# Performance work log

Measured on AMD Instinct MI355X. Metric: run time of the kernel, lower is better.

## Reference

```python
import jax, jax.numpy as jnp
import numpy as np

N = 16384   # total nodes
M = 512     # molecules
D_IN = 64
D_OUT = 64
NEG = -1e9  # mask value for nodes outside a molecule


def setup_inputs() -> dict:
    key = jax.random.key(0)
    ks = jax.random.split(key, 8)
    node_features = jax.random.normal(ks[0], (N, D_IN), dtype=jnp.float32)
    e = jax.random.uniform(ks[1], (N, N), dtype=jnp.float32) * (2.0 / N)
    # molecule membership: sorted segment ids -> one-hot membership matrix
    seg = np.sort(np.asarray(jax.random.randint(ks[2], (N,), 0, M)))
    mnm = (seg[None, :] == np.arange(M)[:, None]).astype(np.float32)
    mol_node_matrix = jnp.asarray(mnm)
    mol_node_mask = jnp.asarray((1.0 - mnm) * NEG)
    s = 1.0 / np.sqrt(D_IN)
    W0 = jax.random.uniform(ks[3], (D_OUT, D_IN), jnp.float32, -s, s)
    b0 = jnp.zeros((D_OUT,), jnp.float32)
    W1 = jax.random.uniform(ks[4], (D_OUT, D_OUT), jnp.float32, -s, s)
    b1 = jnp.zeros((D_OUT,), jnp.float32)
    w2 = jax.random.uniform(ks[5], (1, D_OUT), jnp.float32, -s, s)
    b2 = jnp.zeros((1,), jnp.float32)
    return dict(node_features=node_features, e=e,
                mol_node_matrix=mol_node_matrix, mol_node_mask=mol_node_mask,
                W0=W0, b0=b0, W1=W1, b1=b1, w2=w2, b2=b2)


def reference(node_features, e, mol_node_matrix, mol_node_mask, W0, b0, W1, b1, w2, b2):
    # GraphConvolutionLayer: two linears with adjacency matmul, LeakyReLU between
    h = e @ (node_features @ W0.T + b0)            # [N, D_OUT]
    h = jax.nn.leaky_relu(h, negative_slope=0.01)
    h = e @ (h @ W1.T + b1)                        # [N, D_OUT]
    h = jnp.tanh(h)
    # attention logits per node; mol_node_matrix @ diag(a) == mnm * a^T (broadcast)
    a = (h @ w2.T + b2).reshape(-1)                # [N]
    logits = mol_node_matrix * a[None, :] + mol_node_mask  # [M, N]
    mol_node_weight = jax.nn.softmax(logits, axis=1)
    return mol_node_weight @ h, mol_node_weight
```

## Files before the change

kernel.cpp:

```cpp
#include <hip/hip_runtime.h>
#include <hip/hip_bf16.h>

#define NN 16384
#define MM 512
#define DD 64
#define BK 128
#define BM 32
#define ITERS (NN / BK)
#define BK2 256
#define ITERS2 (NN / BK2)

typedef __attribute__((ext_vector_type(8))) short short8;
typedef __attribute__((ext_vector_type(4))) float f32x4;
typedef __attribute__((ext_vector_type(4))) short short4v;
typedef __attribute__((ext_vector_type(4))) unsigned u32x4;

#define SE 2097152.0f
#define INV_SE 4.76837158203125e-07f

__device__ __forceinline__ short f2bf(float f) {
  union { __hip_bfloat16 b; short s; } u;
  u.b = __float2bfloat16(f);
  return u.s;
}

__device__ __forceinline__ short8 cvt8(f32x4 a, f32x4 b) {
  short8 r;
  r[0] = f2bf(a[0]); r[1] = f2bf(a[1]); r[2] = f2bf(a[2]); r[3] = f2bf(a[3]);
  r[4] = f2bf(b[0]); r[5] = f2bf(b[1]); r[6] = f2bf(b[2]); r[7] = f2bf(b[3]);
  return r;
}

typedef __attribute__((address_space(1))) const unsigned gu32;
typedef __attribute__((address_space(3))) unsigned lu32;
__device__ __forceinline__ void gld16(const void* g, void* l) {
  __builtin_amdgcn_global_load_lds((gu32*)g, (lu32*)l, 16, 0, 0);
}

template <int OFMT>
__global__ __launch_bounds__(256) void linear_mfma(const float* __restrict__ in,
                                                   const float* __restrict__ W,
                                                   const float* __restrict__ b,
                                                   void* __restrict__ xt_) {
  const int t = threadIdx.x, lane = t & 63, w = t >> 6;
  const int rl = lane & 15, hi = lane >> 4;
  const int r0 = blockIdx.x * 64 + w * 16;
  const float* ap = in + (size_t)(r0 + rl) * DD + hi * 8;

  f32x4 acc[4];
#pragma unroll
  for (int g = 0; g < 4; ++g) {
    const float bias = b[g * 16 + rl];
    acc[g][0] = bias; acc[g][1] = bias; acc[g][2] = bias; acc[g][3] = bias;
  }
#pragma unroll
  for (int kk = 0; kk < DD; kk += 32) {
    const short8 af = cvt8(*(const f32x4*)(ap + kk), *(const f32x4*)(ap + kk + 4));
#pragma unroll
    for (int g = 0; g < 4; ++g) {
      const float* wp = W + (size_t)(g * 16 + rl) * DD + hi * 8 + kk;
      const short8 wf = cvt8(*(const f32x4*)wp, *(const f32x4*)(wp + 4));
      acc[g] = __builtin_amdgcn_mfma_f32_16x16x32_bf16(af, wf, acc[g], 0, 0, 0);
    }
  }
#pragma unroll
  for (int g = 0; g < 4; ++g) {
    if (OFMT == 0) {
      unsigned short* xt = (unsigned short*)xt_;
      short4v s;
      s[0] = f2bf(acc[g][0]); s[1] = f2bf(acc[g][1]);
      s[2] = f2bf(acc[g][2]); s[3] = f2bf(acc[g][3]);
      *(short4v*)(xt + (size_t)(g * 16 + rl) * NN + r0 + hi * 4) = s;
    } else {
      unsigned char* xt = (unsigned char*)xt_;
      int pk = __builtin_amdgcn_cvt_pk_fp8_f32(acc[g][0], acc[g][1], 0, false);
      pk = __builtin_amdgcn_cvt_pk_fp8_f32(acc[g][2], acc[g][3], pk, true);
      *(unsigned*)(xt + (size_t)(g * 16 + rl) * NN + r0 + hi * 4) = (unsigned)pk;
    }
  }
}

__global__ __launch_bounds__(256) void gemm1(const float* __restrict__ e,
                                             const unsigned short* __restrict__ xt,
                                             float* __restrict__ out,
                                             unsigned char* __restrict__ e8) {
  __shared__ float Ab[2][BM * BK];
  __shared__ unsigned short Bb[2][64 * BK];
  const int t = threadIdx.x, lane = t & 63, w = t >> 6;
  const int rl = lane & 15, hi = lane >> 4;
  const int wr = w >> 1, wc = w & 1;
  const int r0 = blockIdx.x * BM;
  const int it0 = (blockIdx.x * 37) & (ITERS - 1);

  auto STAGE = [&](int buf, int it) {
    const int k0 = ((it0 + it) & (ITERS - 1)) * BK;
#pragma unroll
    for (int j = 0; j < 4; ++j) {
      const int row = w * 8 + j * 2 + (lane >> 5);
      const float* src =
          e + (size_t)(r0 + row) * NN + k0 + (((lane & 31) ^ (row & 7)) << 2);
      gld16(src, &Ab[buf][(w * 8 + j * 2) * BK]);
    }
#pragma unroll
    for (int j = 0; j < 4; ++j) {
      const int col = w * 16 + j * 4 + (lane >> 4);
      const unsigned short* src =
          xt + (size_t)col * NN + k0 + (((lane & 15) ^ (col & 7)) << 3);
      gld16(src, &Bb[buf][(w * 16 + j * 4) * BK]);
    }
  };

  f32x4 acc[2];
  acc[0][0] = acc[0][1] = acc[0][2] = acc[0][3] = 0.f;
  acc[1][0] = acc[1][1] = acc[1][2] = acc[1][3] = 0.f;

  STAGE(0, 0);
#pragma unroll 1
  for (int it = 0; it < ITERS; ++it) {
    const int cur = it & 1;
    const int k0c = ((it0 + it) & (ITERS - 1)) * BK;
    if (it + 1 < ITERS) {
      STAGE(cur ^ 1, it + 1);
      asm volatile("s_waitcnt vmcnt(9)" ::: "memory");
    } else {
      asm volatile("s_waitcnt vmcnt(0)" ::: "memory");
    }
    __builtin_amdgcn_s_barrier();
    asm volatile("" ::: "memory");
    {
      const int r = t >> 3, j0 = t & 7;
      const float* arow = &Ab[cur][r * BK];
      u32x4 dw;
#pragma unroll
      for (int i = 0; i < 4; ++i) {
        const int c = j0 * 4 + i;
        f32x4 q = *(const f32x4*)&arow[(c ^ (r & 7)) << 2];
        int d = __builtin_amdgcn_cvt_pk_fp8_f32(q[0] * SE, q[1] * SE, 0, false);
        d = __builtin_amdgcn_cvt_pk_fp8_f32(q[2] * SE, q[3] * SE, d, true);
        dw[i] = (unsigned)d;
      }
      *(u32x4*)(e8 + (size_t)(r0 + r) * NN + k0c + j0 * 16) = dw;
    }
#pragma unroll
    for (int kk = 0; kk < BK; kk += 32) {
      const int ca = (kk >> 2) + hi * 2;
      const int arow = (wr * 16 + rl) * BK;
      f32x4 a0 = *(const f32x4*)&Ab[cur][arow + ((ca ^ (rl & 7)) << 2)];
      f32x4 a1 = *(const f32x4*)&Ab[cur][arow + (((ca + 1) ^ (rl & 7)) << 2)];
      const short8 af = cvt8(a0, a1);
      const int cb = (kk >> 3) + hi;
#pragma unroll
      for (int g = 0; g < 2; ++g) {
        const int col = wc * 32 + g * 16 + rl;
        const short8 bf =
            *(const short8*)&Bb[cur][col * BK + ((cb ^ (rl & 7)) << 3)];
        acc[g] = __builtin_amdgcn_mfma_f32_16x16x32_bf16(af, bf, acc[g], 0, 0, 0);
      }
    }
    asm volatile("" ::: "memory");
    __builtin_amdgcn_s_barrier();
  }

#pragma unroll
  for (int g = 0; g < 2; ++g) {
    const int col = wc * 32 + g * 16 + rl;
#pragma unroll
    for (int j = 0; j < 4; ++j) {
      float v = acc[g][j];
      v = (v > 0.f) ? v : 0.01f * v;
      out[(size_t)(r0 + wr * 16 + hi * 4 + j) * DD + col] = v;
    }
  }
}

__global__ __launch_bounds__(256) void gemm2_fp8(const unsigned char* __restrict__ e8,
                                                 const unsigned char* __restrict__ xt8,
                                                 float* __restrict__ out) {
  __shared__ unsigned char Ab2[2][BM * BK2];
  __shared__ unsigned char Bb2[2][64 * BK2];
  const int t = threadIdx.x, lane = t & 63, w = t >> 6;
  const int rl = lane & 15, hi = lane >> 4;
  const int wr = w >> 1, wc = w & 1;
  const int r0 = blockIdx.x * BM;
  const int it0 = (blockIdx.x * 37) & (ITERS2 - 1);

  auto STAGE = [&](int buf, int it) {
    const int k0 = ((it0 + it) & (ITERS2 - 1)) * BK2;
#pragma unroll
    for (int j = 0; j < 2; ++j) {
      const int row = w * 8 + j * 4 + (lane >> 4);
      const unsigned char* src =
          e8 + (size_t)(r0 + row) * NN + k0 + (((lane & 15) ^ (row & 15)) << 4);
      gld16(src, &Ab2[buf][(w * 8 + j * 4) * BK2]);
    }
#pragma unroll
    for (int j = 0; j < 4; ++j) {
      const int col = w * 16 + j * 4 + (lane >> 4);
      const unsigned char* src =
          xt8 + (size_t)col * NN + k0 + (((lane & 15) ^ (col & 15)) << 4);
      gld16(src, &Bb2[buf][(w * 16 + j * 4) * BK2]);
    }
  };

  f32x4 acc[2];
  acc[0][0] = acc[0][1] = acc[0][2] = acc[0][3] = 0.f;
  acc[1][0] = acc[1][1] = acc[1][2] = acc[1][3] = 0.f;

  STAGE(0, 0);
#pragma unroll 1
  for (int it = 0; it < ITERS2; ++it) {
    const int cur = it & 1;
    if (it + 1 < ITERS2) {
      STAGE(cur ^ 1, it + 1);
      asm volatile("s_waitcnt vmcnt(6)" ::: "memory");
    } else {
      asm volatile("s_waitcnt vmcnt(0)" ::: "memory");
    }
    __builtin_amdgcn_s_barrier();
    asm volatile("" ::: "memory");
    const unsigned char* arow = &Ab2[cur][(wr * 16 + rl) * BK2];
#pragma unroll
    for (int kk = 0; kk < BK2; kk += 32) {
      const int ca = (kk >> 4) + (hi >> 1);
      const int off = (hi & 1) * 8;
      const long af = *(const long*)&arow[((ca ^ (rl & 15)) << 4) + off];
#pragma unroll
      for (int g = 0; g < 2; ++g) {
        const int col = wc * 32 + g * 16 + rl;
        const long bf =
            *(const long*)&Bb2[cur][col * BK2 + ((ca ^ (col & 15)) << 4) + off];
        acc[g] = __builtin_amdgcn_mfma_f32_16x16x32_fp8_fp8(af, bf, acc[g], 0, 0, 0);
      }
    }
    asm volatile("" ::: "memory");
    __builtin_amdgcn_s_barrier();
  }

#pragma unroll
  for (int g = 0; g < 2; ++g) {
    const int col = wc * 32 + g * 16 + rl;
#pragma unroll
    for (int j = 0; j < 4; ++j) {
      float v = tanhf(acc[g][j] * INV_SE);
      out[(size_t)(r0 + wr * 16 + hi * 4 + j) * DD + col] = v;
    }
  }
}

__global__ __launch_bounds__(256) void a_kernel(const float* __restrict__ h,
                                                const float* __restrict__ w2,
                                                const float* __restrict__ b2,
                                                float* __restrict__ a) {
  const int t = threadIdx.x;
  const int lane = t & 63;
  const int n = blockIdx.x * 4 + (t >> 6);
  float v = h[(size_t)n * DD + lane] * w2[lane];
#pragma unroll
  for (int off = 32; off > 0; off >>= 1) v += __shfl_xor(v, off);
  if (lane == 0) a[n] = v + b2[0];
}

__global__ __launch_bounds__(256) void softmax_pool(const float* __restrict__ mnm,
                                                    const float* __restrict__ a,
                                                    const float* __restrict__ h,
                                                    float* __restrict__ wout,
                                                    float* __restrict__ out0) {
  __shared__ float red[256];
  __shared__ int redi[256];
  __shared__ float partial[4][64];
  const int m = blockIdx.x, t = threadIdx.x;
  const size_t base = (size_t)m * NN;
  const f32x4* mnm4 = (const f32x4*)(mnm + base);
  const f32x4* a4 = (const f32x4*)a;
  f32x4* wout4 = (f32x4*)(wout + base);

  f32x4 lg[16];
  float mx = -3.0e38f;
  int mn_n = NN, mx_n = -1;
#pragma unroll
  for (int i = 0; i < 16; ++i) {
    const int idx = t + i * 256;
    const f32x4 mv = mnm4[idx];
    const f32x4 av = a4[idx];
    f32x4 v;
#pragma unroll
    for (int j = 0; j < 4; ++j) {
      const bool mem = mv[j] > 0.5f;
      v[j] = mem ? av[j] : -3.0e38f;
      if (mem) {
        const int n = idx * 4 + j;
        mn_n = min(mn_n, n);
        mx_n = max(mx_n, n);
      }
    }
    lg[i] = v;
    mx = fmaxf(mx, fmaxf(fmaxf(v[0], v[1]), fmaxf(v[2], v[3])));
  }
  red[t] = mx; redi[t] = mn_n; __syncthreads();
  for (int s = 128; s > 0; s >>= 1) {
    if (t < s) {
      red[t] = fmaxf(red[t], red[t + s]);
      redi[t] = min(redi[t], redi[t + s]);
    }
    __syncthreads();
  }
  mx = red[0];
  const int ns = redi[0];
  __syncthreads();
  redi[t] = mx_n; __syncthreads();
  for (int s = 128; s > 0; s >>= 1) {
    if (t < s) redi[t] = max(redi[t], redi[t + s]);
    __syncthreads();
  }
  const int ne = redi[0];
  __syncthreads();

  const bool empty = (ne < 0);
  float sm = 0.f;
#pragma unroll
  for (int i = 0; i < 16; ++i) {
    f32x4 v = lg[i];
#pragma unroll
    for (int j = 0; j < 4; ++j)
      v[j] = empty ? 1.0f : ((v[j] > -1.0e38f) ? expf(v[j] - mx) : 0.0f);
    lg[i] = v;
    sm += v[0] + v[1] + v[2] + v[3];
  }
  red[t] = sm; __syncthreads();
  for (int s = 128; s > 0; s >>= 1) {
    if (t < s) red[t] += red[t + s];
    __syncthreads();
  }
  const float inv = 1.0f / red[0];
#pragma unroll
  for (int i = 0; i < 16; ++i) wout4[t + i * 256] = lg[i] * inv;

  __threadfence_block();
  __syncthreads();

  const int s0 = empty ? 0 : ns;
  const int e0 = empty ? NN : ne + 1;
  const int d = t & 63, sub = t >> 6;
  const float* wrow = wout + base;
  float accp = 0.f;
  for (int n = s0 + sub; n < e0; n += 4)
    accp += wrow[n] * h[(size_t)n * DD + d];
  partial[sub][d] = accp;
  __syncthreads();
  if (t < 64)
    out0[m * DD + t] =
        partial[0][t] + partial[1][t] + partial[2][t] + partial[3][t];
}

extern "C" void kernel_launch(void* const* d_in, const int* in_sizes, int n_in,
                              void* d_out, int out_size, void* d_ws, size_t ws_size,
                              hipStream_t stream) {
  const float* nf  = (const float*)d_in[0];
  const float* e   = (const float*)d_in[1];
  const float* mnm = (const float*)d_in[2];
  const float* W0  = (const float*)d_in[4];
  const float* b0  = (const float*)d_in[5];
  const float* W1  = (const float*)d_in[6];
  const float* b1  = (const float*)d_in[7];
  const float* w2  = (const float*)d_in[8];
  const float* b2  = (const float*)d_in[9];

  char* ws = (char*)d_ws;
  unsigned short* XT0 = (unsigned short*)(ws);
  unsigned char*  XT8 = (unsigned char*)(ws + (size_t)2 * 1024 * 1024);
  float* h1 = (float*)(ws + (size_t)4 * 1024 * 1024);
  float* h  = (float*)(ws + (size_t)8 * 1024 * 1024);
  float* av = (float*)(ws + (size_t)12 * 1024 * 1024);
  unsigned char* e8 = (unsigned char*)(ws + (size_t)16 * 1024 * 1024);

  float* out0 = (float*)d_out;
  float* wout = out0 + (size_t)MM * DD;

  linear_mfma<0><<<256, 256, 0, stream>>>(nf, W0, b0, XT0);
  gemm1<<<512, 256, 0, stream>>>(e, XT0, h1, e8);
  linear_mfma<1><<<256, 256, 0, stream>>>(h1, W1, b1, XT8);
  gemm2_fp8<<<512, 256, 0, stream>>>(e8, XT8, h);
  a_kernel<<<4096, 256, 0, stream>>>(h, w2, b2, av);
  softmax_pool<<<512, 256, 0, stream>>>(mnm, av, h, wout, out0);
}
```

Measured before the change: 383.9 us.

## Load B operand directly from global into registers, bypassing LDS

Both adjacency GEMM kernels stop staging the small transposed B matrix (xt / xt8) through shared memory. Each wave now loads its MFMA B fragments straight from global memory into double-buffered registers, with the loop unrolled by two to alternate register buffers. This removes LDS traffic and shared memory for B, which may raise occupancy. In exchange it adds register pressure, non-coalesced 16/8-byte global loads, and depends on hand-tuned vmcnt wait counts.

```diff
diff --git a/kernel.cpp b/kernel.cpp
--- a/kernel.cpp
+++ b/kernel.cpp
@@ -85,14 +85,16 @@
                                              float* __restrict__ out,
                                              unsigned char* __restrict__ e8) {
   __shared__ float Ab[2][BM * BK];
-  __shared__ unsigned short Bb[2][64 * BK];
   const int t = threadIdx.x, lane = t & 63, w = t >> 6;
   const int rl = lane & 15, hi = lane >> 4;
   const int wr = w >> 1, wc = w & 1;
   const int r0 = blockIdx.x * BM;
   const int it0 = (blockIdx.x * 37) & (ITERS - 1);
 
-  auto STAGE = [&](int buf, int it) {
+  const unsigned short* bp0 = xt + (size_t)(wc * 32 + rl) * NN + hi * 8;
+  const unsigned short* bp1 = xt + (size_t)(wc * 32 + 16 + rl) * NN + hi * 8;
+
+  auto STAGE_A = [&](int buf, int it) {
     const int k0 = ((it0 + it) & (ITERS - 1)) * BK;
 #pragma unroll
     for (int j = 0; j < 4; ++j) {
@@ -101,12 +103,15 @@
           e + (size_t)(r0 + row) * NN + k0 + (((lane & 31) ^ (row & 7)) << 2);
       gld16(src, &Ab[buf][(w * 8 + j * 2) * BK]);
     }
-#pragma unroll
-    for (int j = 0; j < 4; ++j) {
-      const int col = w * 16 + j * 4 + (lane >> 4);
-      const unsigned short* src =
-          xt + (size_t)col * NN + k0 + (((lane & 15) ^ (col & 7)) << 3);
-      gld16(src, &Bb[buf][(w * 16 + j * 4) * BK]);
+  };
+
+  short8 bA[8], bB[8];
+  auto LOADB = [&](short8* dst, int it) {
+    const int k0 = ((it0 + it) & (ITERS - 1)) * BK;
+#pragma unroll
+    for (int kki = 0; kki < 4; ++kki) {
+      dst[kki] = *(const short8*)(bp0 + k0 + kki * 32);
+      dst[4 + kki] = *(const short8*)(bp1 + k0 + kki * 32);
     }
   };
 
@@ -114,52 +119,52 @@
   acc[0][0] = acc[0][1] = acc[0][2] = acc[0][3] = 0.f;
   acc[1][0] = acc[1][1] = acc[1][2] = acc[1][3] = 0.f;
 
-  STAGE(0, 0);
+#define G1BODY(CUR, BCUR, BNXT, IT)                                            \
+  {                                                                            \
+    const int k0c = ((it0 + (IT)) & (ITERS - 1)) * BK;                         \
+    if ((IT) + 1 < ITERS) {                                                    \
+      STAGE_A((CUR) ^ 1, (IT) + 1);                                            \
+      LOADB(BNXT, (IT) + 1);                                                   \
+      asm volatile("s_waitcnt vmcnt(12)" ::: "memory");                        \
+    } else {                                                                   \
+      asm volatile("s_waitcnt vmcnt(0)" ::: "memory");                         \
+    }                                                                          \
+    __builtin_amdgcn_s_barrier();                                              \
+    asm volatile("" ::: "memory");                                             \
+    {                                                                          \
+      const int r = t >> 3, j0 = t & 7;                                        \
+      const float* arw = &Ab[CUR][r * BK];                                     \
+      u32x4 dw;                                                                \
+      _Pragma("unroll") for (int i = 0; i < 4; ++i) {                          \
+        const int c = j0 * 4 + i;                                              \
+        f32x4 q = *(const f32x4*)&arw[(c ^ (r & 7)) << 2];                     \
+        int d2 = __builtin_amdgcn_cvt_pk_fp8_f32(q[0] * SE, q[1] * SE, 0, false); \
+        d2 = __builtin_amdgcn_cvt_pk_fp8_f32(q[2] * SE, q[3] * SE, d2, true);  \
+        dw[i] = (unsigned)d2;                                                  \
+      }                                                                        \
+      *(u32x4*)(e8 + (size_t)(r0 + r) * NN + k0c + j0 * 16) = dw;              \
+    }                                                                          \
+    _Pragma("unroll") for (int kk = 0; kk < BK; kk += 32) {                    \
+      const int ca = (kk >> 2) + hi * 2;                                       \
+      const int arow = (wr * 16 + rl) * BK;                                    \
+      f32x4 a0 = *(const f32x4*)&Ab[CUR][arow + ((ca ^ (rl & 7)) << 2)];       \
+      f32x4 a1 = *(const f32x4*)&Ab[CUR][arow + (((ca + 1) ^ (rl & 7)) << 2)]; \
+      const short8 af = cvt8(a0, a1);                                          \
+      acc[0] = __builtin_amdgcn_mfma_f32_16x16x32_bf16(af, (BCUR)[kk >> 5], acc[0], 0, 0, 0);     \
+      acc[1] = __builtin_amdgcn_mfma_f32_16x16x32_bf16(af, (BCUR)[4 + (kk >> 5)], acc[1], 0, 0, 0); \
+    }                                                                          \
+    asm volatile("" ::: "memory");                                             \
+    __builtin_amdgcn_s_barrier();                                              \
+  }
+
+  STAGE_A(0, 0);
+  LOADB(bA, 0);
 #pragma unroll 1
-  for (int it = 0; it < ITERS; ++it) {
-    const int cur = it & 1;
-    const int k0c = ((it0 + it) & (ITERS - 1)) * BK;
-    if (it + 1 < ITERS) {
-      STAGE(cur ^ 1, it + 1);
-      asm volatile("s_waitcnt vmcnt(9)" ::: "memory");
-    } else {
-      asm volatile("s_waitcnt vmcnt(0)" ::: "memory");
-    }
-    __builtin_amdgcn_s_barrier();
-    asm volatile("" ::: "memory");
-    {
-      const int r = t >> 3, j0 = t & 7;
-      const float* arow = &Ab[cur][r * BK];
-      u32x4 dw;
-#pragma unroll
-      for (int i = 0; i < 4; ++i) {
-        const int c = j0 * 4 + i;
-        f32x4 q = *(const f32x4*)&arow[(c ^ (r & 7)) << 2];
-        int d = __builtin_amdgcn_cvt_pk_fp8_f32(q[0] * SE, q[1] * SE, 0, false);
-        d = __builtin_amdgcn_cvt_pk_fp8_f32(q[2] * SE, q[3] * SE, d, true);
-        dw[i] = (unsigned)d;
-      }
-      *(u32x4*)(e8 + (size_t)(r0 + r) * NN + k0c + j0 * 16) = dw;
-    }
-#pragma unroll
-    for (int kk = 0; kk < BK; kk += 32) {
-      const int ca = (kk >> 2) + hi * 2;
-      const int arow = (wr * 16 + rl) * BK;
-      f32x4 a0 = *(const f32x4*)&Ab[cur][arow + ((ca ^ (rl & 7)) << 2)];
-      f32x4 a1 = *(const f32x4*)&Ab[cur][arow + (((ca + 1) ^ (rl & 7)) << 2)];
-      const short8 af = cvt8(a0, a1);
-      const int cb = (kk >> 3) + hi;
-#pragma unroll
-      for (int g = 0; g < 2; ++g) {
-        const int col = wc * 32 + g * 16 + rl;
-        const short8 bf =
-            *(const short8*)&Bb[cur][col * BK + ((cb ^ (rl & 7)) << 3)];
-        acc[g] = __builtin_amdgcn_mfma_f32_16x16x32_bf16(af, bf, acc[g], 0, 0, 0);
-      }
-    }
-    asm volatile("" ::: "memory");
-    __builtin_amdgcn_s_barrier();
-  }
+  for (int it = 0; it < ITERS; it += 2) {
+    G1BODY(0, bA, bB, it);
+    G1BODY(1, bB, bA, it + 1);
+  }
+#undef G1BODY
 
 #pragma unroll
   for (int g = 0; g < 2; ++g) {
@@ -177,14 +182,16 @@
                                                  const unsigned char* __restrict__ xt8,
                                                  float* __restrict__ out) {
   __shared__ unsigned char Ab2[2][BM * BK2];
-  __shared__ unsigned char Bb2[2][64 * BK2];
   const int t = threadIdx.x, lane = t & 63, w = t >> 6;
   const int rl = lane & 15, hi = lane >> 4;
   const int wr = w >> 1, wc = w & 1;
   const int r0 = blockIdx.x * BM;
   const int it0 = (blockIdx.x * 37) & (ITERS2 - 1);
 
-  auto STAGE = [&](int buf, int it) {
+  const unsigned char* bq0 = xt8 + (size_t)(wc * 32 + rl) * NN + hi * 8;
+  const unsigned char* bq1 = xt8 + (size_t)(wc * 32 + 16 + rl) * NN + hi * 8;
+
+  auto STAGE_A = [&](int buf, int it) {
     const int k0 = ((it0 + it) & (ITERS2 - 1)) * BK2;
 #pragma unroll
     for (int j = 0; j < 2; ++j) {
@@ -193,12 +200,15 @@
           e8 + (size_t)(r0 + row) * NN + k0 + (((lane & 15) ^ (row & 15)) << 4);
       gld16(src, &Ab2[buf][(w * 8 + j * 4) * BK2]);
     }
-#pragma unroll
-    for (int j = 0; j < 4; ++j) {
-      const int col = w * 16 + j * 4 + (lane >> 4);
-      const unsigned char* src =
-          xt8 + (size_t)col * NN + k0 + (((lane & 15) ^ (col & 15)) << 4);
-      gld16(src, &Bb2[buf][(w * 16 + j * 4) * BK2]);
+  };
+
+  long bA[16], bB[16];
+  auto LOADB = [&](long* dst, int it) {
+    const int k0 = ((it0 + it) & (ITERS2 - 1)) * BK2;
+#pragma unroll
+    for (int kki = 0; kki < 8; ++kki) {
+      dst[kki] = *(const long*)(bq0 + k0 + kki * 32);
+      dst[8 + kki] = *(const long*)(bq1 + k0 + kki * 32);
     }
   };
 
@@ -206,35 +216,37 @@
   acc[0][0] = acc[0][1] = acc[0][2] = acc[0][3] = 0.f;
   acc[1][0] = acc[1][1] = acc[1][2] = acc[1][3] = 0.f;
 
-  STAGE(0, 0);
+#define G2BODY(CUR, BCUR, BNXT, IT)                                            \
+  {                                                                            \
+    if ((IT) + 1 < ITERS2) {                                                   \
+      STAGE_A((CUR) ^ 1, (IT) + 1);                                            \
+      LOADB(BNXT, (IT) + 1);                                                   \
+      asm volatile("s_waitcnt vmcnt(18)" ::: "memory");                        \
+    } else {                                                                   \
+      asm volatile("s_waitcnt vmcnt(0)" ::: "memory");                         \
+    }                                                                          \
+    __builtin_amdgcn_s_barrier();                                              \
+    asm volatile("" ::: "memory");                                             \
+    const unsigned char* arw = &Ab2[CUR][(wr * 16 + rl) * BK2];                \
+    _Pragma("unroll") for (int kk = 0; kk < BK2; kk += 32) {                   \
+      const int ca = (kk >> 4) + (hi >> 1);                                    \
+      const int off = (hi & 1) * 8;                                            \
+      const long af = *(const long*)&arw[((ca ^ (rl & 15)) << 4) + off];       \
+      acc[0] = __builtin_amdgcn_mfma_f32_16x16x32_fp8_fp8(af, (BCUR)[kk >> 5], acc[0], 0, 0, 0);      \
+      acc[1] = __builtin_amdgcn_mfma_f32_16x16x32_fp8_fp8(af, (BCUR)[8 + (kk >> 5)], acc[1], 0, 0, 0); \
+    }                                                                          \
+    asm volatile("" ::: "memory");                                             \
+    __builtin_amdgcn_s_barrier();                                              \
+  }
+
+  STAGE_A(0, 0);
+  LOADB(bA, 0);
 #pragma unroll 1
-  for (int it = 0; it < ITERS2; ++it) {
-    const int cur = it & 1;
-    if (it + 1 < ITERS2) {
-      STAGE(cur ^ 1, it + 1);
-      asm volatile("s_waitcnt vmcnt(6)" ::: "memory");
-    } else {
-      asm volatile("s_waitcnt vmcnt(0)" ::: "memory");
-    }
-    __builtin_amdgcn_s_barrier();
-    asm volatile("" ::: "memory");
-    const unsigned char* arow = &Ab2[cur][(wr * 16 + rl) * BK2];
-#pragma unroll
-    for (int kk = 0; kk < BK2; kk += 32) {
-      const int ca = (kk >> 4) + (hi >> 1);
-      const int off = (hi & 1) * 8;
-      const long af = *(const long*)&arow[((ca ^ (rl & 15)) << 4) + off];
-#pragma unroll
-      for (int g = 0; g < 2; ++g) {
-        const int col = wc * 32 + g * 16 + rl;
-        const long bf =
-            *(const long*)&Bb2[cur][col * BK2 + ((ca ^ (col & 15)) << 4) + off];
-        acc[g] = __builtin_amdgcn_mfma_f32_16x16x32_fp8_fp8(af, bf, acc[g], 0, 0, 0);
-      }
-    }
-    asm volatile("" ::: "memory");
-    __builtin_amdgcn_s_barrier();
-  }
+  for (int it = 0; it < ITERS2; it += 2) {
+    G2BODY(0, bA, bB, it);
+    G2BODY(1, bB, bA, it + 1);
+  }
+#undef G2BODY
 
 #pragma unroll
   for (int g = 0; g < 2; ++g) {
```

After: 619.4 us. 61.3% more time.

## Halve row tile to 16 and double grid for both adjacency GEMMs

Applied to the files above, without the earlier changes.

Shrinks the per-block row tile of both large GEMMs from 32 to 16 rows. Each of the four waves now owns one 16-column slice, and the grid grows from 512 to 1024 blocks, so there are more blocks than the 256 CUs can hold at once and more waves to hide memory latency. Staging, the fp8 conversion of e, the wait counts and the epilogue are all re-mapped to match. The cost is that the B operand (the XT matrix) is reloaded twice as often across blocks, and each wave issues fewer MFMAs per barrier.

```diff
diff --git a/kernel.cpp b/kernel.cpp
--- a/kernel.cpp
+++ b/kernel.cpp
@@ -5,7 +5,7 @@
 #define MM 512
 #define DD 64
 #define BK 128
-#define BM 32
+#define BM 16
 #define ITERS (NN / BK)
 #define BK2 256
 #define ITERS2 (NN / BK2)
@@ -13,7 +13,7 @@
 typedef __attribute__((ext_vector_type(8))) short short8;
 typedef __attribute__((ext_vector_type(4))) float f32x4;
 typedef __attribute__((ext_vector_type(4))) short short4v;
-typedef __attribute__((ext_vector_type(4))) unsigned u32x4;
+typedef __attribute__((ext_vector_type(2))) unsigned u32x2;
 
 #define SE 2097152.0f
 #define INV_SE 4.76837158203125e-07f
@@ -88,18 +88,17 @@
   __shared__ unsigned short Bb[2][64 * BK];
   const int t = threadIdx.x, lane = t & 63, w = t >> 6;
   const int rl = lane & 15, hi = lane >> 4;
-  const int wr = w >> 1, wc = w & 1;
   const int r0 = blockIdx.x * BM;
   const int it0 = (blockIdx.x * 37) & (ITERS - 1);
 
   auto STAGE = [&](int buf, int it) {
     const int k0 = ((it0 + it) & (ITERS - 1)) * BK;
 #pragma unroll
-    for (int j = 0; j < 4; ++j) {
-      const int row = w * 8 + j * 2 + (lane >> 5);
+    for (int j = 0; j < 2; ++j) {
+      const int row = w * 4 + j * 2 + (lane >> 5);
       const float* src =
           e + (size_t)(r0 + row) * NN + k0 + (((lane & 31) ^ (row & 7)) << 2);
-      gld16(src, &Ab[buf][(w * 8 + j * 2) * BK]);
+      gld16(src, &Ab[buf][(w * 4 + j * 2) * BK]);
     }
 #pragma unroll
     for (int j = 0; j < 4; ++j) {
@@ -110,9 +109,8 @@
     }
   };
 
-  f32x4 acc[2];
-  acc[0][0] = acc[0][1] = acc[0][2] = acc[0][3] = 0.f;
-  acc[1][0] = acc[1][1] = acc[1][2] = acc[1][3] = 0.f;
+  f32x4 acc;
+  acc[0] = acc[1] = acc[2] = acc[3] = 0.f;
 
   STAGE(0, 0);
 #pragma unroll 1
@@ -121,54 +119,50 @@
     const int k0c = ((it0 + it) & (ITERS - 1)) * BK;
     if (it + 1 < ITERS) {
       STAGE(cur ^ 1, it + 1);
-      asm volatile("s_waitcnt vmcnt(9)" ::: "memory");
+      asm volatile("s_waitcnt vmcnt(6)" ::: "memory");
     } else {
       asm volatile("s_waitcnt vmcnt(0)" ::: "memory");
     }
     __builtin_amdgcn_s_barrier();
     asm volatile("" ::: "memory");
     {
-      const int r = t >> 3, j0 = t & 7;
-      const float* arow = &Ab[cur][r * BK];
-      u32x4 dw;
-#pragma unroll
-      for (int i = 0; i < 4; ++i) {
-        const int c = j0 * 4 + i;
-        f32x4 q = *(const f32x4*)&arow[(c ^ (r & 7)) << 2];
-        int d = __builtin_amdgcn_cvt_pk_fp8_f32(q[0] * SE, q[1] * SE, 0, false);
-        d = __builtin_amdgcn_cvt_pk_fp8_f32(q[2] * SE, q[3] * SE, d, true);
-        dw[i] = (unsigned)d;
+      const int r = t >> 4, j0 = t & 15;
+      const float* arw = &Ab[cur][r * BK];
+      u32x2 dw;
+#pragma unroll
+      for (int i = 0; i < 2; ++i) {
+        const int c = j0 * 2 + i;
+        f32x4 q = *(const f32x4*)&arw[(c ^ (r & 7)) << 2];
+        int d2 = __builtin_amdgcn_cvt_pk_fp8_f32(q[0] * SE, q[1] * SE, 0, false);
+        d2 = __builtin_amdgcn_cvt_pk_fp8_f32(q[2] * SE, q[3] * SE, d2, true);
+        dw[i] = (unsigned)d2;
       }
-      *(u32x4*)(e8 + (size_t)(r0 + r) * NN + k0c + j0 * 16) = dw;
+      *(u32x2*)(e8 + (size_t)(r0 + r) * NN + k0c + j0 * 8) = dw;
     }
 #pragma unroll
     for (int kk = 0; kk < BK; kk += 32) {
       const int ca = (kk >> 2) + hi * 2;
-      const int arow = (wr * 16 + rl) * BK;
+      const int arow = rl * BK;
       f32x4 a0 = *(const f32x4*)&Ab[cur][arow + ((ca ^ (rl & 7)) << 2)];
       f32x4 a1 = *(const f32x4*)&Ab[cur][arow + (((ca + 1) ^ (rl & 7)) << 2)];
       const short8 af = cvt8(a0, a1);
       const int cb = (kk >> 3) + hi;
-#pragma unroll
-      for (int g = 0; g < 2; ++g) {
-        const int col = wc * 32 + g * 16 + rl;
-        const short8 bf =
-            *(const short8*)&Bb[cur][col * BK + ((cb ^ (rl & 7)) << 3)];
-        acc[g] = __builtin_amdgcn_mfma_f32_16x16x32_bf16(af, bf, acc[g], 0, 0, 0);
-      }
+      const int col = w * 16 + rl;
+      const short8 bf =
+          *(const short8*)&Bb[cur][col * BK + ((cb ^ (rl & 7)) << 3)];
+      acc = __builtin_amdgcn_mfma_f32_16x16x32_bf16(af, bf, acc, 0, 0, 0);
     }
     asm volatile("" ::: "memory");
     __builtin_amdgcn_s_barrier();
   }
 
-#pragma unroll
-  for (int g = 0; g < 2; ++g) {
-    const int col = wc * 32 + g * 16 + rl;
-#pragma unroll
-    for (int j = 0; j < 4; ++j) {
-      float v = acc[g][j];
+  {
+    const int col = w * 16 + rl;
+#pragma unroll
+    for (int j = 0; j < 4; ++j) {
+      float v = acc[j];
       v = (v > 0.f) ? v : 0.01f * v;
-      out[(size_t)(r0 + wr * 16 + hi * 4 + j) * DD + col] = v;
+      out[(size_t)(r0 + hi * 4 + j) * DD + col] = v;
     }
   }
 }
@@ -180,18 +174,16 @@
   __shared__ unsigned char Bb2[2][64 * BK2];
   const int t = threadIdx.x, lane = t & 63, w = t >> 6;
   const int rl = lane & 15, hi = lane >> 4;
-  const int wr = w >> 1, wc = w & 1;
   const int r0 = blockIdx.x * BM;
   const int it0 = (blockIdx.x * 37) & (ITERS2 - 1);
 
   auto STAGE = [&](int buf, int it) {
     const int k0 = ((it0 + it) & (ITERS2 - 1)) * BK2;
-#pragma unroll
-    for (int j = 0; j < 2; ++j) {
-      const int row = w * 8 + j * 4 + (lane >> 4);
+    {
+      const int row = w * 4 + (lane >> 4);
       const unsigned char* src =
           e8 + (size_t)(r0 + row) * NN + k0 + (((lane & 15) ^ (row & 15)) << 4);
-      gld16(src, &Ab2[buf][(w * 8 + j * 4) * BK2]);
+      gld16(src, &Ab2[buf][w * 4 * BK2]);
     }
 #pragma unroll
     for (int j = 0; j < 4; ++j) {
@@ -202,9 +194,8 @@
     }
   };
 
-  f32x4 acc[2];
-  acc[0][0] = acc[0][1] = acc[0][2] = acc[0][3] = 0.f;
-  acc[1][0] = acc[1][1] = acc[1][2] = acc[1][3] = 0.f;
+  f32x4 acc;
+  acc[0] = acc[1] = acc[2] = acc[3] = 0.f;
 
   STAGE(0, 0);
 #pragma unroll 1
@@ -212,37 +203,33 @@
     const int cur = it & 1;
     if (it + 1 < ITERS2) {
       STAGE(cur ^ 1, it + 1);
-      asm volatile("s_waitcnt vmcnt(6)" ::: "memory");
+      asm volatile("s_waitcnt vmcnt(5)" ::: "memory");
     } else {
       asm volatile("s_waitcnt vmcnt(0)" ::: "memory");
     }
     __builtin_amdgcn_s_barrier();
     asm volatile("" ::: "memory");
-    const unsigned char* arow = &Ab2[cur][(wr * 16 + rl) * BK2];
+    const unsigned char* arw = &Ab2[cur][rl * BK2];
 #pragma unroll
     for (int kk = 0; kk < BK2; kk += 32) {
       const int ca = (kk >> 4) + (hi >> 1);
       const int off = (hi & 1) * 8;
-      const long af = *(const long*)&arow[((ca ^ (rl & 15)) << 4) + off];
-#pragma unroll
-      for (int g = 0; g < 2; ++g) {
-        const int col = wc * 32 + g * 16 + rl;
-        const long bf =
-            *(const long*)&Bb2[cur][col * BK2 + ((ca ^ (col & 15)) << 4) + off];
-        acc[g] = __builtin_amdgcn_mfma_f32_16x16x32_fp8_fp8(af, bf, acc[g], 0, 0, 0);
-      }
+      const long af = *(const long*)&arw[((ca ^ (rl & 15)) << 4) + off];
+      const int col = w * 16 + rl;
+      const long bf =
+          *(const long*)&Bb2[cur][col * BK2 + ((ca ^ (rl & 15)) << 4) + off];
+      acc = __builtin_amdgcn_mfma_f32_16x16x32_fp8_fp8(af, bf, acc, 0, 0, 0);
     }
     asm volatile("" ::: "memory");
     __builtin_amdgcn_s_barrier();
   }
 
-#pragma unroll
-  for (int g = 0; g < 2; ++g) {
-    const int col = wc * 32 + g * 16 + rl;
-#pragma unroll
-    for (int j = 0; j < 4; ++j) {
-      float v = tanhf(acc[g][j] * INV_SE);
-      out[(size_t)(r0 + wr * 16 + hi * 4 + j) * DD + col] = v;
+  {
+    const int col = w * 16 + rl;
+#pragma unroll
+    for (int j = 0; j < 4; ++j) {
+      float v = tanhf(acc[j] * INV_SE);
+      out[(size_t)(r0 + hi * 4 + j) * DD + col] = v;
     }
   }
 }
@@ -377,9 +364,9 @@
   float* wout = out0 + (size_t)MM * DD;
 
   linear_mfma<0><<<256, 256, 0, stream>>>(nf, W0, b0, XT0);
-  gemm1<<<512, 256, 0, stream>>>(e, XT0, h1, e8);
+  gemm1<<<1024, 256, 0, stream>>>(e, XT0, h1, e8);
   linear_mfma<1><<<256, 256, 0, stream>>>(h1, W1, b1, XT8);
-  gemm2_fp8<<<512, 256, 0, stream>>>(e8, XT8, h);
+  gemm2_fp8<<<1024, 256, 0, stream>>>(e8, XT8, h);
   a_kernel<<<4096, 256, 0, stream>>>(h, w2, b2, av);
   softmax_pool<<<512, 256, 0, stream>>>(mnm, av, h, wout, out0);
 }
```

After: 488.6 us. +27.3%, slower.
